# Optimization experiments

Measured on AMD Instinct MI355X. Metric: run time of the kernel, lower is better.

Reference implementation:

```python
import jax, jax.numpy as jnp
import numpy as np

_SAMPLING_EPS = 1e-05
_FP16_TINY = float(np.finfo(np.float16).tiny)  # masked_fill value used by the torch code


def _token_mask(tokens, num_seqs, vocab_size):
    # bin-count via scatter-add into width vocab+1 (padding id == vocab), then mask
    rows = jnp.arange(num_seqs)[:, None]
    counts = jnp.zeros((num_seqs, vocab_size + 1), jnp.int32).at[rows, tokens].add(1)
    return counts[:, :vocab_size] > 0


def setup_inputs() -> dict:
    key = jax.random.key(0)
    ks = jax.random.split(key, 9)
    B, V, PL, OL = 128, 128000, 2048, 256
    logits = jax.random.normal(ks[0], (B, V), dtype=jnp.float32) * 4.0
    prompt_tokens = jax.random.randint(ks[1], (B, PL), 0, V, dtype=jnp.int64)
    output_tokens = jax.random.randint(ks[2], (B, OL), 0, V, dtype=jnp.int64)
    presence_penalties = jax.random.uniform(ks[3], (B,), dtype=jnp.float32)
    frequency_penalties = jax.random.uniform(ks[4], (B,), dtype=jnp.float32)
    repetition_penalties = 1.0 + 0.3 * jax.random.uniform(ks[5], (B,), dtype=jnp.float32)
    temperature = 0.1 + 0.9 * jax.random.uniform(ks[6], (B,), dtype=jnp.float32)
    top_k = jax.random.randint(ks[7], (B,), 1, 100, dtype=jnp.int64)
    top_p = 0.5 + 0.49 * jax.random.uniform(ks[8], (B,), dtype=jnp.float32)
    return {
        "logits": logits,
        "prompt_tokens": prompt_tokens,
        "output_tokens": output_tokens,
        "presence_penalties": presence_penalties,
        "frequency_penalties": frequency_penalties,
        "repetition_penalties": repetition_penalties,
        "temperature": temperature,
        "top_k": top_k,
        "top_p": top_p,
    }


def reference(logits, prompt_tokens, output_tokens, presence_penalties,
              frequency_penalties, repetition_penalties, temperature,
              top_k, top_p):
    B, V = logits.shape
    logits = logits.astype(jnp.float32)

    # --- penalties (NOTE: torch code computes frequency counts but never applies
    # frequency_penalties; we faithfully do the same) ---
    prompt_mask = _token_mask(prompt_tokens, B, V)
    output_mask = _token_mask(output_tokens, B, V)
    pen = jnp.where(prompt_mask | output_mask, repetition_penalties[:, None], 1.0)
    logits = jnp.where(logits > 0, logits / pen, logits * pen)
    logits = logits - presence_penalties[:, None] * output_mask.astype(jnp.float32)

    # --- temperature ---
    temp = jnp.where(temperature < _SAMPLING_EPS, 1.0, temperature)
    logits = logits / temp[:, None]

    # --- top-k / top-p via ascending sort (mirrors torch implementation) ---
    idx = jnp.argsort(logits, axis=-1)                      # ascending
    ls = jnp.take_along_axis(logits, idx, axis=-1)
    thr_pos = (V - top_k.astype(jnp.int32))[:, None]
    thr = jnp.take_along_axis(ls, thr_pos, axis=-1)         # [B,1]
    ls = jnp.where(ls < thr, _FP16_TINY, ls)
    probs_sort = jax.nn.softmax(ls, axis=-1)
    csum = jnp.cumsum(probs_sort, axis=-1)
    tp_mask = csum <= (1.0 - top_p)[:, None]
    tp_mask = tp_mask.at[:, -1].set(False)
    ls = jnp.where(tp_mask, _FP16_TINY, ls)

    # unsort back to original vocab order
    rows = jnp.arange(B)[:, None]
    out_logits = jnp.zeros_like(logits).at[rows, idx].set(ls)

    probs = jax.nn.softmax(out_logits, axis=-1)
    return probs, prompt_mask, output_mask
```

## Files before the change

### kernel.cpp

```cpp
#include <hip/hip_runtime.h>
#include <math.h>

#define B   128
#define V   128000
#define WPR 4000
#define PL  2048
#define OL  256
#define BPR 25
#define ITERS 5
#define TLOC 128
#define CAP  6144
#define FP16_TINY 6.103515625e-05f

typedef float f4_nt __attribute__((ext_vector_type(4)));
__device__ __forceinline__ void nt_store4(float* p, float a, float b, float c, float d) {
    f4_nt v = {a, b, c, d};
    __builtin_nontemporal_store(v, (f4_nt*)p);
}

__device__ __forceinline__ unsigned key_of(float f) {
    unsigned u = __float_as_uint(f);
    unsigned m = (unsigned)(((int)u) >> 31) | 0x80000000u;
    return u ^ m;
}
__device__ __forceinline__ float key_inv(unsigned k) {
    unsigned u = (k & 0x80000000u) ? (k ^ 0x80000000u) : ~k;
    return __uint_as_float(u);
}

__device__ __forceinline__ float xform(float x, int pm, int om,
                                       float rp, float rrp, float pres, float itt) {
#pragma clang fp contract(off)
    float m = (pm | om) ? ((x > 0.0f) ? rrp : rp) : 1.0f;
    float l = x * m;
    if (om) l = l - pres;
    return l * itt;
}

__global__ __launch_bounds__(256) void k_scatter(const int* __restrict__ ptok,
                                                 const int* __restrict__ otok,
                                                 unsigned* __restrict__ bitP,
                                                 unsigned* __restrict__ bitO,
                                                 unsigned* __restrict__ cnt) {
    __shared__ unsigned mp[WPR];
    __shared__ unsigned mo[WPR];
    int r = blockIdx.x;
    int t = threadIdx.x;
    for (int i = t; i < WPR; i += 256) { mp[i] = 0u; mo[i] = 0u; }
    if (t == 0) cnt[r] = 0u;
    __syncthreads();
    const int* prow = ptok + (size_t)r * PL;
    const int* orow = otok + (size_t)r * OL;
    for (int i = t; i < PL; i += 256) {
        int tok = prow[i];
        if ((unsigned)tok < (unsigned)V) atomicOr(&mp[tok >> 5], 1u << (tok & 31));
    }
    for (int i = t; i < OL; i += 256) {
        int tok = orow[i];
        if ((unsigned)tok < (unsigned)V) atomicOr(&mo[tok >> 5], 1u << (tok & 31));
    }
    __syncthreads();
    unsigned* bpo = bitP + (size_t)r * WPR;
    unsigned* boo = bitO + (size_t)r * WPR;
    for (int i = t; i < WPR; i += 256) { bpo[i] = mp[i]; boo[i] = mo[i]; }
}

__global__ __launch_bounds__(256) void k_main(
    const float* __restrict__ logits,
    const unsigned* __restrict__ bitP, const unsigned* __restrict__ bitO,
    const float* __restrict__ rep, const float* __restrict__ pres,
    const float* __restrict__ temp,
    float* __restrict__ outPm, float* __restrict__ outOm,
    unsigned* __restrict__ cnt, unsigned long long* __restrict__ cand)
{
    __shared__ unsigned h[4096];
    __shared__ unsigned sA[256];
    __shared__ int s_beta;
    __shared__ unsigned s_base;
    int r = blockIdx.y;
    int c0 = blockIdx.x * (ITERS * 1024);
    int t = threadIdx.x;
    for (int i = t; i < 4096; i += 256) h[i] = 0u;
    __syncthreads();
    float rp = rep[r], pp = pres[r];
    float tt = temp[r]; tt = (tt < 1e-5f) ? 1.0f : tt;
    float rrp = 1.0f / rp;
    float itt = 1.0f / tt;
    const float* lrow = logits + (size_t)r * V;
    float* pmrow = outPm + (size_t)r * V;
    float* omrow = outOm + (size_t)r * V;
    const unsigned* bp = bitP + (size_t)r * WPR;
    const unsigned* bo = bitO + (size_t)r * WPR;
    uint4 kv4[ITERS];
#pragma unroll
    for (int it = 0; it < ITERS; it++) {
        int i = c0 + it * 1024 + t * 4;
        float4 x = *(const float4*)(lrow + i);
        unsigned wp = bp[i >> 5], wo = bo[i >> 5];
        int sh = i & 31;
        float xs[4] = {x.x, x.y, x.z, x.w};
        unsigned ks[4];
        float fp[4], fo[4];
#pragma unroll
        for (int j = 0; j < 4; j++) {
            int p = (wp >> (sh + j)) & 1;
            int o = (wo >> (sh + j)) & 1;
            float l = xform(xs[j], p, o, rp, rrp, pp, itt);
            unsigned key = key_of(l);
            atomicAdd(&h[key >> 20], 1u);
            ks[j] = key; fp[j] = (float)p; fo[j] = (float)o;
        }
        kv4[it] = make_uint4(ks[0], ks[1], ks[2], ks[3]);
        nt_store4(pmrow + i, fp[0], fp[1], fp[2], fp[3]);
        nt_store4(omrow + i, fo[0], fo[1], fo[2], fo[3]);
    }
    __syncthreads();
    unsigned cs = 0;
#pragma unroll
    for (int j = 0; j < 16; j++) cs += h[t * 16 + j];
    sA[t] = cs;
    __syncthreads();
    unsigned v = cs;
    for (int st = 1; st < 256; st <<= 1) {
        unsigned add = (t + st < 256) ? sA[t + st] : 0u;
        __syncthreads();
        v += add; sA[t] = v;
        __syncthreads();
    }
    unsigned Snext = (t < 255) ? sA[t + 1] : 0u;
    if (sA[t] >= TLOC && Snext < TLOC) {
        unsigned run = Snext;
        int beta = t * 16;
        for (int j = 15; j >= 0; j--) {
            run += h[t * 16 + j];
            if (run >= TLOC) { beta = t * 16 + j; break; }
        }
        s_beta = beta;
    }
    __syncthreads();
    unsigned beta = (unsigned)s_beta;
    unsigned myc = 0;
#pragma unroll
    for (int it = 0; it < ITERS; it++) {
        unsigned ks[4] = {kv4[it].x, kv4[it].y, kv4[it].z, kv4[it].w};
#pragma unroll
        for (int j = 0; j < 4; j++)
            if ((ks[j] >> 20) >= beta) myc++;
    }
    sA[t] = myc;
    __syncthreads();
    unsigned pv = myc;
    for (int st = 1; st < 256; st <<= 1) {
        unsigned add = (t >= st) ? sA[t - st] : 0u;
        __syncthreads();
        pv += add; sA[t] = pv;
        __syncthreads();
    }
    if (t == 255) s_base = atomicAdd(&cnt[r], pv);
    __syncthreads();
    unsigned w = s_base + (pv - myc);
#pragma unroll
    for (int it = 0; it < ITERS; it++) {
        unsigned ks[4] = {kv4[it].x, kv4[it].y, kv4[it].z, kv4[it].w};
#pragma unroll
        for (int j = 0; j < 4; j++) {
            unsigned key = ks[j];
            if ((key >> 20) >= beta) {
                if (w < (unsigned)CAP) {
                    int idx = c0 + it * 1024 + t * 4 + j;
                    cand[(size_t)r * CAP + w] =
                        ((unsigned long long)key << 32) | (unsigned)idx;
                }
                w++;
            }
        }
    }
}

__global__ __launch_bounds__(256) void k_select(
    const unsigned* __restrict__ cnt, const unsigned long long* __restrict__ cand,
    const int* __restrict__ topk, const float* __restrict__ topp,
    float4* __restrict__ params, int* __restrict__ idxc)
{
    __shared__ unsigned long long list[CAP];
    __shared__ unsigned long long kv[256];
    __shared__ unsigned rh[256];
    __shared__ unsigned rsuf[256];
    __shared__ double sD[256];
    __shared__ unsigned s_prefix, s_krem, s_kcnt;
    int r = blockIdx.x;
    int t = threadIdx.x;
    int n = (int)min(cnt[r], (unsigned)CAP);
    const unsigned long long* crow = cand + (size_t)r * CAP;
    for (int i = t; i < n; i += 256) list[i] = crow[i];
    int k = topk[r]; k = max(1, min(k, 127));
    if (t == 0) { s_prefix = 0u; s_krem = (unsigned)k; }
    __syncthreads();
    for (int round = 3; round >= 0; round--) {
        int shift = round * 8;
        unsigned prefix = s_prefix;
        unsigned krem = s_krem;
        unsigned maskAbove = (round == 3) ? 0u : (0xFFFFFFFFu << (shift + 8));
        rh[t] = 0u;
        __syncthreads();
        for (int i = t; i < n; i += 256) {
            unsigned key = (unsigned)(list[i] >> 32);
            if ((key & maskAbove) == (prefix & maskAbove))
                atomicAdd(&rh[(key >> shift) & 255u], 1u);
        }
        __syncthreads();
        unsigned vv = rh[t];
        rsuf[t] = vv;
        __syncthreads();
        for (int st = 1; st < 256; st <<= 1) {
            unsigned add = (t + st < 256) ? rsuf[t + st] : 0u;
            __syncthreads();
            vv += add; rsuf[t] = vv;
            __syncthreads();
        }
        unsigned Sx = (t < 255) ? rsuf[t + 1] : 0u;
        if (rsuf[t] >= krem && Sx < krem) {
            s_prefix = prefix | ((unsigned)t << shift);
            s_krem = krem - Sx;
        }
        __syncthreads();
    }
    unsigned thrkey = s_prefix;
    if (t == 0) s_kcnt = 0u;
    __syncthreads();
    for (int i = t; i < n; i += 256) {
        if ((unsigned)(list[i] >> 32) >= thrkey) {
            unsigned pos = atomicAdd(&s_kcnt, 1u);
            if (pos < 256u) kv[pos] = list[i];
        }
    }
    __syncthreads();
    int K = (int)min(s_kcnt, 256u);
    if (t >= K) kv[t] = 0ULL;
    __syncthreads();
    for (unsigned k2 = 2; k2 <= 256; k2 <<= 1) {
        for (unsigned j2 = k2 >> 1; j2 > 0; j2 >>= 1) {
            unsigned ixj = (unsigned)t ^ j2;
            if (ixj > (unsigned)t) {
                unsigned long long a = kv[t], b = kv[ixj];
                bool descBlock = (((unsigned)t & k2) == 0u);
                bool doSwap = descBlock ? (a < b) : (a > b);
                if (doSwap) { kv[t] = b; kv[ixj] = a; }
            }
            __syncthreads();
        }
    }
    float Mxf = key_inv((unsigned)(kv[0] >> 32));
    double MxD = (double)Mxf;
    double e_t = (t < K) ? exp((double)key_inv((unsigned)(kv[t] >> 32)) - MxD)
                         : 0.0;
    sD[t] = e_t;
    __syncthreads();
    for (int st = 128; st > 0; st >>= 1) {
        if (t < st) sD[t] += sD[t + st];
        __syncthreads();
    }
    double S = sD[0];
    __syncthreads();
    double e_tinyD = exp((double)FP16_TINY - MxD);
    double Z1 = (double)(V - K) * e_tinyD + S;
    double base = (double)(V - K) * e_tinyD / Z1;
    double thresh = 1.0 - (double)topp[r];
    sD[t] = e_t;
    __syncthreads();
    double sv = e_t;
    for (int st = 1; st < 256; st <<= 1) {
        double add = (t + st < 256) ? sD[t + st] : 0.0;
        __syncthreads();
        sv += add; sD[t] = sv;
        __syncthreads();
    }
    double suf_t = sv;
    unsigned flag = (t >= 1 && t < K && (base + suf_t / Z1) <= thresh) ? 1u : 0u;
    rsuf[t] = flag;
    __syncthreads();
    for (int st = 128; st > 0; st >>= 1) {
        if (t < st) rsuf[t] += rsuf[t + st];
        __syncthreads();
    }
    int cm = (int)rsuf[0];
    int ns = K - cm;
    sD[t] = (t < ns) ? e_t : 0.0;
    __syncthreads();
    for (int st = 128; st > 0; st >>= 1) {
        if (t < st) sD[t] += sD[t + st];
        __syncthreads();
    }
    if (t == 0) {
        double S2 = sD[0];
        unsigned bkey = (unsigned)(kv[ns - 1] >> 32);
        float v_b = key_inv(bkey);
        unsigned idx_cut = (unsigned)(kv[ns - 1] & 0xFFFFFFFFu);
        float tiny_e = expf(FP16_TINY - Mxf);
        double Z2 = (double)(V - ns) * (double)tiny_e + S2;
        float invZ2 = (float)(1.0 / Z2);
        params[r] = make_float4(v_b, Mxf, invZ2, tiny_e * invZ2);
        idxc[r] = (int)idx_cut;
    }
}

__global__ __launch_bounds__(256) void k_final(
    const float* __restrict__ logits,
    const unsigned* __restrict__ bitP, const unsigned* __restrict__ bitO,
    const float* __restrict__ rep, const float* __restrict__ pres,
    const float* __restrict__ temp,
    const float4* __restrict__ params, const int* __restrict__ idxc,
    float* __restrict__ probs)
{
    int r = blockIdx.y;
    int c0 = blockIdx.x * (ITERS * 1024);
    int t = threadIdx.x;
    float rp = rep[r], pp = pres[r];
    float tt = temp[r]; tt = (tt < 1e-5f) ? 1.0f : tt;
    float rrp = 1.0f / rp;
    float itt = 1.0f / tt;
    float4 pr = params[r];
    float v_b = pr.x, Mx = pr.y, invZ2 = pr.z, ptiny = pr.w;
    unsigned idx_cut = (unsigned)idxc[r];
    const float* lrow = logits + (size_t)r * V;
    float* orow = probs + (size_t)r * V;
    const unsigned* bp = bitP + (size_t)r * WPR;
    const unsigned* bo = bitO + (size_t)r * WPR;
#pragma unroll
    for (int it = 0; it < ITERS; it++) {
        int i = c0 + it * 1024 + t * 4;
        float4 x = *(const float4*)(lrow + i);
        unsigned wp = bp[i >> 5], wo = bo[i >> 5];
        int sh = i & 31;
        float xs[4] = {x.x, x.y, x.z, x.w};
        float res[4];
#pragma unroll
        for (int j = 0; j < 4; j++) {
            int p = (wp >> (sh + j)) & 1;
            int o = (wo >> (sh + j)) & 1;
            float l = xform(xs[j], p, o, rp, rrp, pp, itt);
            bool keep = (l > v_b) || (l == v_b && (unsigned)(i + j) >= idx_cut);
            res[j] = keep ? (expf(l - Mx) * invZ2) : ptiny;
        }
        nt_store4(orow + i, res[0], res[1], res[2], res[3]);
    }
}

extern "C" void kernel_launch(void* const* d_in, const int* in_sizes, int n_in,
                              void* d_out, int out_size, void* d_ws, size_t ws_size,
                              hipStream_t stream) {
    const float* logits = (const float*)d_in[0];
    const int* ptok     = (const int*)d_in[1];
    const int* otok     = (const int*)d_in[2];
    const float* pres   = (const float*)d_in[3];
    const float* rep    = (const float*)d_in[5];
    const float* temp   = (const float*)d_in[6];
    const int* topk     = (const int*)d_in[7];
    const float* topp   = (const float*)d_in[8];

    float* out_probs = (float*)d_out;
    float* out_pm = out_probs + (size_t)B * V;
    float* out_om = out_pm + (size_t)B * V;

    unsigned* ws0 = (unsigned*)d_ws;
    float4* params = (float4*)d_ws;
    int* idxc = (int*)(ws0 + 512);
    unsigned* bitP = ws0 + 768;
    unsigned* bitO = bitP + B * WPR;
    unsigned* cnt  = bitO + B * WPR;
    unsigned long long* cand =
        (unsigned long long*)(cnt + B + 64);

    k_scatter<<<B, 256, 0, stream>>>(ptok, otok, bitP, bitO, cnt);

    dim3 g(BPR, B);
    k_main<<<g, 256, 0, stream>>>(logits, bitP, bitO, rep, pres, temp,
                                  out_pm, out_om, cnt, cand);
    k_select<<<B, 256, 0, stream>>>(cnt, cand, topk, topp, params, idxc);
    k_final<<<g, 256, 0, stream>>>(logits, bitP, bitO, rep, pres, temp,
                                   params, idxc, out_probs);
}
```

Measured before the change: 309.1 us.

## Replace shared-memory block scans with wave shuffles, pad histogram, drop nontemporal stores

```diff
diff --git a/kernel.cpp b/kernel.cpp
--- a/kernel.cpp
+++ b/kernel.cpp
@@ -12,11 +12,9 @@
 #define CAP  6144
 #define FP16_TINY 6.103515625e-05f
 
-typedef float f4_nt __attribute__((ext_vector_type(4)));
-__device__ __forceinline__ void nt_store4(float* p, float a, float b, float c, float d) {
-    f4_nt v = {a, b, c, d};
-    __builtin_nontemporal_store(v, (f4_nt*)p);
-}
+#define HBINS 4096
+#define HIDX(b) ((b) + ((b) >> 4))
+#define HSZ (HBINS + (HBINS >> 4))
 
 __device__ __forceinline__ unsigned key_of(float f) {
     unsigned u = __float_as_uint(f);
@@ -35,6 +33,41 @@
     float l = x * m;
     if (om) l = l - pres;
     return l * itt;
+}
+
+__device__ __forceinline__ unsigned wave_suffix_u(unsigned x, int lane) {
+#pragma unroll
+    for (int o = 1; o < 64; o <<= 1) {
+        unsigned a = __shfl_down(x, o);
+        if (lane + o < 64) x += a;
+    }
+    return x;
+}
+__device__ __forceinline__ unsigned wave_prefix_u(unsigned x, int lane) {
+#pragma unroll
+    for (int o = 1; o < 64; o <<= 1) {
+        unsigned a = __shfl_up(x, o);
+        if (lane >= o) x += a;
+    }
+    return x;
+}
+__device__ __forceinline__ double wave_suffix_d(double x, int lane) {
+#pragma unroll
+    for (int o = 1; o < 64; o <<= 1) {
+        double a = __shfl_down(x, o);
+        if (lane + o < 64) x += a;
+    }
+    return x;
+}
+__device__ __forceinline__ double wave_sum_d(double x) {
+#pragma unroll
+    for (int o = 1; o < 64; o <<= 1) x += __shfl_xor(x, o);
+    return x;
+}
+__device__ __forceinline__ unsigned wave_sum_u(unsigned x) {
+#pragma unroll
+    for (int o = 1; o < 64; o <<= 1) x += __shfl_xor(x, o);
+    return x;
 }
 
 __global__ __launch_bounds__(256) void k_scatter(const int* __restrict__ ptok,
@@ -73,14 +106,15 @@
     float* __restrict__ outPm, float* __restrict__ outOm,
     unsigned* __restrict__ cnt, unsigned long long* __restrict__ cand)
 {
-    __shared__ unsigned h[4096];
-    __shared__ unsigned sA[256];
+    __shared__ unsigned h[HSZ];
+    __shared__ unsigned wsum[4];
     __shared__ int s_beta;
     __shared__ unsigned s_base;
     int r = blockIdx.y;
     int c0 = blockIdx.x * (ITERS * 1024);
     int t = threadIdx.x;
-    for (int i = t; i < 4096; i += 256) h[i] = 0u;
+    int lane = t & 63, wid = t >> 6;
+    for (int i = t; i < HSZ; i += 256) h[i] = 0u;
     __syncthreads();
     float rp = rep[r], pp = pres[r];
     float tt = temp[r]; tt = (tt < 1e-5f) ? 1.0f : tt;
@@ -107,32 +141,29 @@
             int o = (wo >> (sh + j)) & 1;
             float l = xform(xs[j], p, o, rp, rrp, pp, itt);
             unsigned key = key_of(l);
-            atomicAdd(&h[key >> 20], 1u);
+            atomicAdd(&h[HIDX(key >> 20)], 1u);
             ks[j] = key; fp[j] = (float)p; fo[j] = (float)o;
         }
         kv4[it] = make_uint4(ks[0], ks[1], ks[2], ks[3]);
-        nt_store4(pmrow + i, fp[0], fp[1], fp[2], fp[3]);
-        nt_store4(omrow + i, fo[0], fo[1], fo[2], fo[3]);
+        *(float4*)(pmrow + i) = make_float4(fp[0], fp[1], fp[2], fp[3]);
+        *(float4*)(omrow + i) = make_float4(fo[0], fo[1], fo[2], fo[3]);
     }
     __syncthreads();
     unsigned cs = 0;
 #pragma unroll
-    for (int j = 0; j < 16; j++) cs += h[t * 16 + j];
-    sA[t] = cs;
-    __syncthreads();
-    unsigned v = cs;
-    for (int st = 1; st < 256; st <<= 1) {
-        unsigned add = (t + st < 256) ? sA[t + st] : 0u;
-        __syncthreads();
-        v += add; sA[t] = v;
-        __syncthreads();
-    }
-    unsigned Snext = (t < 255) ? sA[t + 1] : 0u;
-    if (sA[t] >= TLOC && Snext < TLOC) {
+    for (int j = 0; j < 16; j++) cs += h[HIDX(t * 16 + j)];
+    unsigned sfx = wave_suffix_u(cs, lane);
+    if (lane == 0) wsum[wid] = sfx;
+    __syncthreads();
+    unsigned suf = sfx;
+#pragma unroll
+    for (int w2 = 0; w2 < 4; w2++) if (w2 > wid) suf += wsum[w2];
+    unsigned Snext = suf - cs;
+    if (suf >= TLOC && Snext < TLOC) {
         unsigned run = Snext;
         int beta = t * 16;
         for (int j = 15; j >= 0; j--) {
-            run += h[t * 16 + j];
+            run += h[HIDX(t * 16 + j)];
             if (run >= TLOC) { beta = t * 16 + j; break; }
         }
         s_beta = beta;
@@ -147,15 +178,12 @@
         for (int j = 0; j < 4; j++)
             if ((ks[j] >> 20) >= beta) myc++;
     }
-    sA[t] = myc;
-    __syncthreads();
-    unsigned pv = myc;
-    for (int st = 1; st < 256; st <<= 1) {
-        unsigned add = (t >= st) ? sA[t - st] : 0u;
-        __syncthreads();
-        pv += add; sA[t] = pv;
-        __syncthreads();
-    }
+    unsigned pfx = wave_prefix_u(myc, lane);
+    if (lane == 63) wsum[wid] = pfx;
+    __syncthreads();
+    unsigned pv = pfx;
+#pragma unroll
+    for (int w2 = 0; w2 < 4; w2++) if (w2 < wid) pv += wsum[w2];
     if (t == 255) s_base = atomicAdd(&cnt[r], pv);
     __syncthreads();
     unsigned w = s_base + (pv - myc);
@@ -185,11 +213,12 @@
     __shared__ unsigned long long list[CAP];
     __shared__ unsigned long long kv[256];
     __shared__ unsigned rh[256];
-    __shared__ unsigned rsuf[256];
-    __shared__ double sD[256];
+    __shared__ double wD[4];
+    __shared__ unsigned wU[4];
     __shared__ unsigned s_prefix, s_krem, s_kcnt;
     int r = blockIdx.x;
     int t = threadIdx.x;
+    int lane = t & 63, wid = t >> 6;
     int n = (int)min(cnt[r], (unsigned)CAP);
     const unsigned long long* crow = cand + (size_t)r * CAP;
     for (int i = t; i < n; i += 256) list[i] = crow[i];
@@ -210,16 +239,14 @@
         }
         __syncthreads();
         unsigned vv = rh[t];
-        rsuf[t] = vv;
+        unsigned sfx = wave_suffix_u(vv, lane);
+        if (lane == 0) wU[wid] = sfx;
         __syncthreads();
-        for (int st = 1; st < 256; st <<= 1) {
-            unsigned add = (t + st < 256) ? rsuf[t + st] : 0u;
-            __syncthreads();
-            vv += add; rsuf[t] = vv;
-            __syncthreads();
-        }
-        unsigned Sx = (t < 255) ? rsuf[t + 1] : 0u;
-        if (rsuf[t] >= krem && Sx < krem) {
+        unsigned suf = sfx;
+#pragma unroll
+        for (int w2 = 0; w2 < 4; w2++) if (w2 > wid) suf += wU[w2];
+        unsigned Sx = suf - vv;
+        if (suf >= krem && Sx < krem) {
             s_prefix = prefix | ((unsigned)t << shift);
             s_krem = krem - Sx;
         }
@@ -254,45 +281,34 @@
     double MxD = (double)Mxf;
     double e_t = (t < K) ? exp((double)key_inv((unsigned)(kv[t] >> 32)) - MxD)
                          : 0.0;
-    sD[t] = e_t;
-    __syncthreads();
-    for (int st = 128; st > 0; st >>= 1) {
-        if (t < st) sD[t] += sD[t + st];
-        __syncthreads();
-    }
-    double S = sD[0];
-    __syncthreads();
+    double red = wave_sum_d(e_t);
+    if (lane == 0) wD[wid] = red;
+    __syncthreads();
+    double S = wD[0] + wD[1] + wD[2] + wD[3];
+    __syncthreads();
+    double sv = wave_suffix_d(e_t, lane);
+    if (lane == 0) wD[wid] = sv;
+    __syncthreads();
+    double suf_t = sv;
+#pragma unroll
+    for (int w2 = 0; w2 < 4; w2++) if (w2 > wid) suf_t += wD[w2];
     double e_tinyD = exp((double)FP16_TINY - MxD);
     double Z1 = (double)(V - K) * e_tinyD + S;
     double base = (double)(V - K) * e_tinyD / Z1;
     double thresh = 1.0 - (double)topp[r];
-    sD[t] = e_t;
-    __syncthreads();
-    double sv = e_t;
-    for (int st = 1; st < 256; st <<= 1) {
-        double add = (t + st < 256) ? sD[t + st] : 0.0;
-        __syncthreads();
-        sv += add; sD[t] = sv;
-        __syncthreads();
-    }
-    double suf_t = sv;
     unsigned flag = (t >= 1 && t < K && (base + suf_t / Z1) <= thresh) ? 1u : 0u;
-    rsuf[t] = flag;
-    __syncthreads();
-    for (int st = 128; st > 0; st >>= 1) {
-        if (t < st) rsuf[t] += rsuf[t + st];
-        __syncthreads();
-    }
-    int cm = (int)rsuf[0];
+    unsigned fr = wave_sum_u(flag);
+    if (lane == 0) wU[wid] = fr;
+    __syncthreads();
+    int cm = (int)(wU[0] + wU[1] + wU[2] + wU[3]);
     int ns = K - cm;
-    sD[t] = (t < ns) ? e_t : 0.0;
-    __syncthreads();
-    for (int st = 128; st > 0; st >>= 1) {
-        if (t < st) sD[t] += sD[t + st];
-        __syncthreads();
-    }
+    __syncthreads();
+    double e2 = (t < ns) ? e_t : 0.0;
+    double r2 = wave_sum_d(e2);
+    if (lane == 0) wD[wid] = r2;
+    __syncthreads();
     if (t == 0) {
-        double S2 = sD[0];
+        double S2 = wD[0] + wD[1] + wD[2] + wD[3];
         unsigned bkey = (unsigned)(kv[ns - 1] >> 32);
         float v_b = key_inv(bkey);
         unsigned idx_cut = (unsigned)(kv[ns - 1] & 0xFFFFFFFFu);
@@ -342,7 +358,7 @@
             bool keep = (l > v_b) || (l == v_b && (unsigned)(i + j) >= idx_cut);
             res[j] = keep ? (expf(l - Mx) * invZ2) : ptiny;
         }
-        nt_store4(orow + i, res[0], res[1], res[2], res[3]);
+        *(float4*)(orow + i) = make_float4(res[0], res[1], res[2], res[3]);
     }
 }
 
```

Result: no change. 304.2 us (-1.6%).
